# Optimization experiments

Hardware: AMD Instinct MI355X
Metric: run time of the kernel (lower is better)

The kernel has to match this reference:

```python
import jax, jax.numpy as jnp
import numpy as np

N, E, D, H, LAYERS = 50000, 800000, 128, 8, 2
LRELU_ALPHA = 0.2


def _seg_softmax(logits, seg, n):
    # numerically stable softmax over edges grouped by destination node
    m = jax.ops.segment_max(logits, seg, num_segments=n)
    z = jnp.exp(logits - m[seg])
    s = jax.ops.segment_sum(z, seg, num_segments=n)
    return z / jnp.maximum(s[seg], 1e-16)


def _gat_layer(x, src, dst, W, a_src, a_dst, concat):
    # W: [H, Fin, F'], a_src/a_dst: [H, F']
    n = x.shape[0]
    outs = []
    for h in range(W.shape[0]):  # loop over heads to bound peak memory
        Wh = x @ W[h]                              # [N, F']
        es = Wh @ a_src[h]                         # [N]
        ed = Wh @ a_dst[h]                         # [N]
        e = jax.nn.leaky_relu(es[src] + ed[dst], LRELU_ALPHA)  # [E]
        att = _seg_softmax(e, dst, n)              # [E]
        out = jax.ops.segment_sum(att[:, None] * Wh[src], dst, num_segments=n)
        outs.append(out)
    if concat:
        return jax.nn.elu(jnp.concatenate(outs, axis=-1))  # [N, H*F']
    return jnp.mean(jnp.stack(outs, axis=0), axis=0)        # [N, F']


def _rel_gcn_layer(x, src, dst, w, W):
    # weighted-adjacency GCN with row (in-degree) normalization + ReLU
    n = x.shape[0]
    deg = jax.ops.segment_sum(w, dst, num_segments=n)
    norm = w / jnp.maximum(deg[dst], 1e-16)        # [E]
    h = x @ W                                      # [N, Dout]
    agg = jax.ops.segment_sum(norm[:, None] * h[src], dst, num_segments=n)
    return jax.nn.relu(agg)


def setup_inputs() -> dict:
    key = jax.random.key(0)
    ks = jax.random.split(key, 12)
    s = 1.0 / np.sqrt(D)
    return {
        "x": jax.random.normal(ks[0], (N, D), dtype=jnp.float32),
        "edge_index": jax.random.randint(ks[1], (2, E), 0, N, dtype=jnp.int64),
        "edge_weight": jax.random.uniform(ks[2], (E,), dtype=jnp.float32),
        "gat_W0": jax.random.normal(ks[3], (H, D, D // H), dtype=jnp.float32) * s,
        "gat_a0_src": jax.random.normal(ks[4], (H, D // H), dtype=jnp.float32) * s,
        "gat_a0_dst": jax.random.normal(ks[5], (H, D // H), dtype=jnp.float32) * s,
        "gat_W1": jax.random.normal(ks[6], (H, D, D), dtype=jnp.float32) * s,
        "gat_a1_src": jax.random.normal(ks[7], (H, D), dtype=jnp.float32) * s,
        "gat_a1_dst": jax.random.normal(ks[8], (H, D), dtype=jnp.float32) * s,
        "gcn_W0": jax.random.normal(ks[9], (D, D), dtype=jnp.float32) * s,
        "gcn_W1": jax.random.normal(ks[10], (D, D), dtype=jnp.float32) * s,
    }


def reference(x, edge_index, edge_weight, gat_W0, gat_a0_src, gat_a0_dst,
              gat_W1, gat_a1_src, gat_a1_dst, gcn_W0, gcn_W1):
    src, dst = edge_index[0], edge_index[1]
    gat_params = [(gat_W0, gat_a0_src, gat_a0_dst), (gat_W1, gat_a1_src, gat_a1_dst)]
    gcn_params = [gcn_W0, gcn_W1]
    x1, x2 = x, x  # dropout is identity in eval mode
    for i in range(LAYERS):
        W, a_s, a_d = gat_params[i]
        x1 = _gat_layer(x1, src, dst, W, a_s, a_d, concat=(i != LAYERS - 1))
        x2 = _rel_gcn_layer(x2, src, dst, edge_weight, gcn_params[i])
    # cat along new last dim then MaxPool1d(2) == elementwise max of branches
    return jnp.maximum(x1, x2)
```

## Files before the change

kernel.cpp:

```cpp
#include <hip/hip_runtime.h>

#define LRELU_ALPHA 0.2f

typedef __attribute__((ext_vector_type(8))) short short8;
typedef __attribute__((ext_vector_type(4))) float float4v;
typedef __attribute__((ext_vector_type(2))) float f32x2;

__device__ __forceinline__ unsigned short f2bf(float f) {
  union { float f; unsigned u; } x; x.f = f;
  unsigned r = (x.u + 0x7fff + ((x.u >> 16) & 1)) >> 16;
  return (unsigned short)r;
}
__device__ __forceinline__ float bflo(unsigned u) {
  union { unsigned u; float f; } x; x.u = u << 16; return x.f;
}
__device__ __forceinline__ float bfhi(unsigned u) {
  union { unsigned u; float f; } x; x.u = u & 0xffff0000u; return x.f;
}
__device__ __forceinline__ f32x2 bfpair(unsigned u) {
  return (f32x2){bflo(u), bfhi(u)};
}


__global__ __launch_bounds__(256) void k_count(const int* __restrict__ dst,
                                               int* __restrict__ cnt, int E) {
  int e = blockIdx.x * 256 + threadIdx.x;
  if (e < E) atomicAdd(&cnt[dst[e]], 1);
}

__global__ __launch_bounds__(1024) void k_scan1(const int* __restrict__ cnt,
                                                int* __restrict__ lscan,
                                                int* __restrict__ bsum, int N) {
  __shared__ int sm[1024];
  int t = threadIdx.x;
  int base = blockIdx.x * 1024;
  int v = (base + t < N) ? cnt[base + t] : 0;
  sm[t] = v;
  __syncthreads();
  for (int off = 1; off < 1024; off <<= 1) {
    int x = (t >= off) ? sm[t - off] : 0;
    __syncthreads();
    sm[t] += x;
    __syncthreads();
  }
  if (base + t < N) lscan[base + t] = sm[t] - v;
  if (t == 1023) bsum[blockIdx.x] = sm[1023];
}

__global__ __launch_bounds__(64) void k_scan2(int* __restrict__ bsum,
                                              int* __restrict__ rowptrN, int nb) {
  int t = threadIdx.x;
  int v = (t < nb) ? bsum[t] : 0;
  int orig = v;
  for (int off = 1; off < 64; off <<= 1) {
    int y = __shfl_up(v, off, 64);
    if (t >= off) v += y;
  }
  if (t < nb) bsum[t] = v - orig;
  if (t == 63) *rowptrN = v;
}

__global__ __launch_bounds__(1024) void k_scan3(int* __restrict__ rowptr,
                                                int* __restrict__ cur,
                                                const int* __restrict__ bsum, int N) {
  int i = blockIdx.x * 1024 + threadIdx.x;
  if (i < N) {
    int v = rowptr[i] + bsum[blockIdx.x];
    rowptr[i] = v;
    cur[i] = v;
  }
}

__global__ __launch_bounds__(256) void k_scatter(const int* __restrict__ src,
                                                 const int* __restrict__ dst,
                                                 const float* __restrict__ w,
                                                 int* __restrict__ cur,
                                                 uint2* __restrict__ edata, int E) {
  int e = blockIdx.x * 256 + threadIdx.x;
  if (e < E) {
    int d = dst[e];
    int p = atomicAdd(&cur[d], 1);
    edata[p] = make_uint2((unsigned)src[e], __float_as_uint(w[e]));
  }
}

__global__ __launch_bounds__(256) void k_pack(const float* __restrict__ W0,
                                              const float* __restrict__ a0s,
                                              const float* __restrict__ a0d,
                                              const float* __restrict__ W1,
                                              const float* __restrict__ a1s,
                                              const float* __restrict__ a1d,
                                              const float* __restrict__ gw0,
                                              const float* __restrict__ gw1,
                                              unsigned short* __restrict__ W0catT,
                                              float* __restrict__ logitW,
                                              unsigned short* __restrict__ gw1T,
                                              unsigned short* __restrict__ va1T,
                                              unsigned short* __restrict__ WstackT) {
  int idx = blockIdx.x * 256 + threadIdx.x;
  if (idx < 32768) {
    int n = idx >> 7, k = idx & 127;
    int q = n >> 2, r = n & 3;
    float v;
    if (r < 2) {
      int o = 2 * q + r;
      int h = o >> 4, f = o & 15;
      v = W0[h * 2048 + k * 16 + f];
    } else {
      int j = 2 * q + (r - 2);
      v = gw0[k * 128 + j];
    }
    W0catT[idx] = f2bf(v);
  } else if (idx < 34816) {
    int j = idx - 32768;
    int k = j >> 4, c = j & 15;
    int h = (c < 8) ? c : c - 8;
    const float* a = (c < 8) ? a0s : a0d;
    float s = 0.f;
    for (int f = 0; f < 16; ++f) s += W0[h * 2048 + k * 16 + f] * a[h * 16 + f];
    logitW[j] = s;
  } else if (idx < 51200) {
    int j = idx - 34816;
    int n = j >> 7, k = j & 127;
    gw1T[j] = f2bf(gw1[k * 128 + n]);
  } else if (idx < 53248) {
    int j = idx - 51200;
    int c = j >> 7, k = j & 127;
    int h = c & 7;
    const float* a = (c < 8) ? a1s : a1d;
    float s = 0.f;
    for (int f = 0; f < 128; ++f) s += W1[h * 16384 + k * 128 + f] * a[h * 128 + f];
    va1T[j] = f2bf(s);
  } else if (idx < 184320) {
    int j = idx - 53248;
    int n = j >> 10, kk = j & 1023;
    int h = kk >> 7, k = kk & 127;
    WstackT[j] = f2bf(W1[h * 16384 + k * 128 + n] * 0.125f);
  }
}

__global__ __launch_bounds__(256) void k_prep(const float* __restrict__ x,
                                              const float* __restrict__ logitW,
                                              unsigned short* __restrict__ xb,
                                              float* __restrict__ logit0, int N) {
  __shared__ float sm[16][132];
  __shared__ float sw[2048];
  int t = threadIdx.x;
  int base = blockIdx.x * 16;
  int r = t >> 4, cc = (t & 15) * 8;
  const float* xr = x + (size_t)(base + r) * 128 + cc;
  float4 v0 = *(const float4*)xr;
  float4 v1 = *(const float4*)(xr + 4);
  ushort4 o0 = {f2bf(v0.x), f2bf(v0.y), f2bf(v0.z), f2bf(v0.w)};
  ushort4 o1 = {f2bf(v1.x), f2bf(v1.y), f2bf(v1.z), f2bf(v1.w)};
  *(ushort4*)(xb + (size_t)(base + r) * 128 + cc) = o0;
  *(ushort4*)(xb + (size_t)(base + r) * 128 + cc + 4) = o1;
  *(float4*)&sm[r][cc] = v0;
  *(float4*)&sm[r][cc + 4] = v1;
  *(float4*)&sw[t * 8] = *(const float4*)(logitW + t * 8);
  *(float4*)&sw[t * 8 + 4] = *(const float4*)(logitW + t * 8 + 4);
  __syncthreads();
  int c = t & 15;
  float acc = 0.f;
#pragma unroll
  for (int k = 0; k < 128; ++k) acc += sm[r][k] * sw[k * 16 + c];
  logit0[(size_t)(base + r) * 16 + c] = acc;
}

__global__ __launch_bounds__(256) void k_pedge(const float* __restrict__ logits,
                                               const uint2* __restrict__ edata,
                                               const int* __restrict__ rowptr,
                                               unsigned short* __restrict__ pedge,
                                               float* __restrict__ linv, int N) {
  int wave = threadIdx.x >> 6, lane = threadIdx.x & 63;
  int d = blockIdx.x * 4 + wave;
  if (d >= N) return;
  int j8 = lane >> 3, h = lane & 7;
  float edv = logits[(size_t)d * 16 + 8 + h];
  int beg = rowptr[d], end = rowptr[d + 1];
  float lsum = 0.f;
  for (int ii = beg + j8; ii < end; ii += 8) {
    unsigned s = edata[ii].x;
    float es = logits[(size_t)s * 16 + h];
    float lg = es + edv;
    lg = lg > 0.f ? lg : LRELU_ALPHA * lg;
    float p = __expf(fminf(lg, 80.f));
    lsum += p;
    pedge[(size_t)ii * 8 + h] = f2bf(p);
  }
  lsum += __shfl_xor(lsum, 8, 64);
  lsum += __shfl_xor(lsum, 16, 64);
  lsum += __shfl_xor(lsum, 32, 64);
  if (lane < 8) linv[(size_t)d * 8 + h] = lsum > 0.f ? 1.f / lsum : 0.f;
}

template <int NT, int OUT_BF16, int EPI>
__global__ __launch_bounds__(256) void k_mgemm(const unsigned short* __restrict__ A, int lda,
                                               const unsigned short* __restrict__ BT, int ldb,
                                               void* __restrict__ Cv, int ldc,
                                               const void* __restrict__ aux,
                                               int M, int Ncols, int K) {
  __shared__ unsigned short As[64][64];
  __shared__ unsigned short Bs[NT * 16][64];
  int tid = threadIdx.x;
  int w = tid >> 6, lane = tid & 63;
  int quad = lane >> 4, l16 = lane & 15;
  int row0 = blockIdx.x * 64;
  int c0 = blockIdx.y * (NT * 16);
  float4v acc[NT];
#pragma unroll
  for (int t = 0; t < NT; ++t) acc[t] = (float4v){0.f, 0.f, 0.f, 0.f};

  for (int k0 = 0; k0 < K; k0 += 64) {
    __syncthreads();
#pragma unroll
    for (int i = 0; i < 2; ++i) {
      int c = tid + i * 256;
      int r = c >> 3, kc = c & 7;
      uint4 v = {0u, 0u, 0u, 0u};
      int gr = row0 + r;
      if (gr < M) v = *(const uint4*)(A + (size_t)gr * lda + k0 + kc * 8);
      *(uint4*)(&As[r][(kc ^ (r & 7)) * 8]) = v;
    }
#pragma unroll
    for (int i = 0; i < (NT * 128 + 255) / 256; ++i) {
      int c = tid + i * 256;
      if (c < NT * 128) {
        int n = c >> 3, kc = c & 7;
        uint4 v = {0u, 0u, 0u, 0u};
        int gn = c0 + n;
        if (gn < Ncols) v = *(const uint4*)(BT + (size_t)gn * ldb + k0 + kc * 8);
        *(uint4*)(&Bs[n][(kc ^ (n & 7)) * 8]) = v;
      }
    }
    __syncthreads();
#pragma unroll
    for (int ks = 0; ks < 2; ++ks) {
      int m = w * 16 + l16;
      int ga = (ks * 4 + quad) ^ (m & 7);
      short8 a = *(const short8*)(&As[m][ga * 8]);
#pragma unroll
      for (int t = 0; t < NT; ++t) {
        int n = t * 16 + l16;
        int gb = (ks * 4 + quad) ^ (n & 7);
        short8 b = *(const short8*)(&Bs[n][gb * 8]);
        acc[t] = __builtin_amdgcn_mfma_f32_16x16x32_bf16(a, b, acc[t], 0, 0, 0);
      }
    }
  }
#pragma unroll
  for (int t = 0; t < NT; ++t) {
    int cc = c0 + t * 16 + l16;
    if (cc >= Ncols) continue;
#pragma unroll
    for (int i = 0; i < 4; ++i) {
      int rr = row0 + w * 16 + quad * 4 + i;
      if (rr >= M) continue;
      float v = acc[t][i];
      if (EPI == 1) {
        unsigned short us = ((const unsigned short*)aux)[(size_t)rr * ldc + cc];
        v = fmaxf(v, bflo((unsigned)us));
      }
      if (EPI == 2) {
        ((unsigned short*)Cv)[(size_t)rr * 256 + 4 * (cc >> 1) + 2 + (cc & 1)] = f2bf(v);
      } else if (OUT_BF16)
        ((unsigned short*)Cv)[(size_t)rr * ldc + cc] = f2bf(v);
      else
        ((float*)Cv)[(size_t)rr * ldc + cc] = v;
    }
  }
}

__global__ __launch_bounds__(256) void k_agg0(const unsigned short* __restrict__ feat0i,
                                              const int* __restrict__ rowptr,
                                              const uint2* __restrict__ edata,
                                              const unsigned short* __restrict__ pedge,
                                              const float* __restrict__ linv,
                                              unsigned short* __restrict__ x1c,
                                              unsigned short* __restrict__ x2,
                                              unsigned short* __restrict__ xh, int N) {
  __shared__ uint2 swl[4][64];
  __shared__ float pl[4][512];
  int wave = threadIdx.x >> 6, lane = threadIdx.x & 63;
  int d = blockIdx.x * 4 + wave;
  if (d >= N) return;
  int head = lane >> 3;
  int beg = rowptr[d], end = rowptr[d + 1], deg = end - beg;
  float wsum = 0.f;
  f32x2 a2 = {0.f, 0.f}, g2 = {0.f, 0.f};
  for (int base = 0; base < deg; base += 64) {
    int idx = beg + base + lane;
    bool valid = idx < end;
    uint2 sv = make_uint2(0u, 0u);
    float4 pa = {0.f, 0.f, 0.f, 0.f}, pb = {0.f, 0.f, 0.f, 0.f};
    if (valid) {
      sv = edata[idx];
      ushort4 q0 = *(const ushort4*)(pedge + (size_t)idx * 8);
      ushort4 q1 = *(const ushort4*)(pedge + (size_t)idx * 8 + 4);
      pa = make_float4(bflo(q0.x), bflo(q0.y), bflo(q0.z), bflo(q0.w));
      pb = make_float4(bflo(q1.x), bflo(q1.y), bflo(q1.z), bflo(q1.w));
    }
    swl[wave][lane] = sv;
    *(float4*)&pl[wave][lane * 8] = pa;
    *(float4*)&pl[wave][lane * 8 + 4] = pb;
    int ng = deg - base; if (ng > 64) ng = 64;
    int groups = (ng + 7) >> 3;
    for (int g = 0; g < groups; ++g) {
#pragma unroll
      for (int j = 0; j < 8; ++j) {
        int e = g * 8 + j;
        uint2 sw = swl[wave][e];
        float pj = pl[wave][e * 8 + head];
        float wj = __uint_as_float(sw.y);
        uint2 u = *(const uint2*)(feat0i + (size_t)sw.x * 256 + 4 * lane);
        a2 += bfpair(u.x) * pj;
        g2 += bfpair(u.y) * wj;
        wsum += wj;
      }
    }
  }
  float inv = linv[(size_t)d * 8 + head];
  float v0 = a2.x * inv, v1 = a2.y * inv;
  v0 = v0 > 0.f ? v0 : __expf(v0) - 1.f;
  v1 = v1 > 0.f ? v1 : __expf(v1) - 1.f;
  unsigned xpack = (unsigned)f2bf(v0) | ((unsigned)f2bf(v1) << 16);
  ((unsigned*)x1c)[(size_t)d * 64 + lane] = xpack;
  ((unsigned*)xh)[(size_t)d * 128 + 2 * lane] = xpack;
  float ginv = 1.f / fmaxf(wsum, 1e-16f);
  float w0 = fmaxf(g2.x * ginv, 0.f), w1 = fmaxf(g2.y * ginv, 0.f);
  ((unsigned*)x2)[(size_t)d * 64 + lane] = (unsigned)f2bf(w0) | ((unsigned)f2bf(w1) << 16);
}

__global__ __launch_bounds__(256) void k_agg1(const unsigned short* __restrict__ xh,
                                              const int* __restrict__ rowptr,
                                              const uint2* __restrict__ edata,
                                              const unsigned short* __restrict__ pedge,
                                              const float* __restrict__ linv,
                                              unsigned short* __restrict__ aggbuf,
                                              unsigned short* __restrict__ x2f,
                                              int d0, int d1) {
  __shared__ uint2 swl[4][64];
  __shared__ float pl[4][512];
  int wave = threadIdx.x >> 6, lane = threadIdx.x & 63;
  int d = d0 + blockIdx.x * 4 + wave;
  if (d >= d1) return;
  int beg = rowptr[d], end = rowptr[d + 1], deg = end - beg;
  f32x2 ax2[8] = {};
  f32x2 g2 = {0.f, 0.f};
  float wsum = 0.f;
  for (int base = 0; base < deg; base += 64) {
    int idx = beg + base + lane;
    bool valid = idx < end;
    uint2 sv = make_uint2(0u, 0u);
    float4 pa = {0.f, 0.f, 0.f, 0.f}, pb = {0.f, 0.f, 0.f, 0.f};
    if (valid) {
      sv = edata[idx];
      ushort4 q0 = *(const ushort4*)(pedge + (size_t)idx * 8);
      ushort4 q1 = *(const ushort4*)(pedge + (size_t)idx * 8 + 4);
      pa = make_float4(bflo(q0.x), bflo(q0.y), bflo(q0.z), bflo(q0.w));
      pb = make_float4(bflo(q1.x), bflo(q1.y), bflo(q1.z), bflo(q1.w));
    }
    swl[wave][lane] = sv;
    *(float4*)&pl[wave][lane * 8] = pa;
    *(float4*)&pl[wave][lane * 8 + 4] = pb;
    int ng = deg - base; if (ng > 64) ng = 64;
    int groups = (ng + 7) >> 3;
    for (int g = 0; g < groups; ++g) {
#pragma unroll
      for (int j = 0; j < 8; ++j) {
        int e = g * 8 + j;
        uint2 sw = swl[wave][e];
        float4 pv0 = *(const float4*)&pl[wave][e * 8];
        float4 pv1 = *(const float4*)&pl[wave][e * 8 + 4];
        uint2 u = *(const uint2*)(xh + (size_t)sw.x * 256 + 4 * lane);
        f32x2 xv = bfpair(u.x);
        float wj = __uint_as_float(sw.y);
        g2 += bfpair(u.y) * wj;
        wsum += wj;
        ax2[0] += xv * pv0.x;
        ax2[1] += xv * pv0.y;
        ax2[2] += xv * pv0.z;
        ax2[3] += xv * pv0.w;
        ax2[4] += xv * pv1.x;
        ax2[5] += xv * pv1.y;
        ax2[6] += xv * pv1.z;
        ax2[7] += xv * pv1.w;
      }
    }
  }
  float4 i0 = *(const float4*)(linv + (size_t)d * 8);
  float4 i1 = *(const float4*)(linv + (size_t)d * 8 + 4);
  float invh[8] = {i0.x, i0.y, i0.z, i0.w, i1.x, i1.y, i1.z, i1.w};
  size_t lr = (size_t)(d - d0) * 512;
#pragma unroll
  for (int h = 0; h < 8; ++h) {
    ((unsigned*)aggbuf)[lr + h * 64 + lane] =
        (unsigned)f2bf(ax2[h].x * invh[h]) | ((unsigned)f2bf(ax2[h].y * invh[h]) << 16);
  }
  float ginv = 1.f / fmaxf(wsum, 1e-16f);
  float w0 = fmaxf(g2.x * ginv, 0.f), w1 = fmaxf(g2.y * ginv, 0.f);
  ((unsigned*)x2f)[(size_t)d * 64 + lane] = (unsigned)f2bf(w0) | ((unsigned)f2bf(w1) << 16);
}


extern "C" void kernel_launch(void* const* d_in, const int* in_sizes, int n_in,
                              void* d_out, int out_size, void* d_ws, size_t ws_size,
                              hipStream_t stream) {
  const float* x   = (const float*)d_in[0];
  const int*   ei  = (const int*)d_in[1];
  const float* ew  = (const float*)d_in[2];
  const float* W0  = (const float*)d_in[3];
  const float* a0s = (const float*)d_in[4];
  const float* a0d = (const float*)d_in[5];
  const float* W1  = (const float*)d_in[6];
  const float* a1s = (const float*)d_in[7];
  const float* a1d = (const float*)d_in[8];
  const float* gw0 = (const float*)d_in[9];
  const float* gw1 = (const float*)d_in[10];
  float* out = (float*)d_out;

  const int N = in_sizes[0] / 128;
  const int E = in_sizes[1] / 2;
  const int* src = ei;
  const int* dst = ei + E;

  char* p = (char*)d_ws;
  auto carve = [&](size_t bytes) {
    void* r = (void*)p;
    p += (bytes + 255) & ~(size_t)255;
    return r;
  };
  int*   cnt    = (int*)carve((size_t)N * 4);
  int*   rowptr = (int*)carve((size_t)(N + 1) * 4);
  int*   cur    = (int*)carve((size_t)N * 4);
  int*   bsum   = (int*)carve(256 * 4);
  uint2* edata  = (uint2*)carve((size_t)E * 8);
  unsigned short* W0catT  = (unsigned short*)carve(32768 * 2);
  float*          logitW  = (float*)carve(2048 * 4);
  unsigned short* gw1T    = (unsigned short*)carve(16384 * 2);
  unsigned short* va1T    = (unsigned short*)carve(2048 * 2);
  unsigned short* WstackT = (unsigned short*)carve(131072 * 2);
  unsigned short* x1c  = (unsigned short*)carve((size_t)N * 128 * 2);
  unsigned short* x2   = (unsigned short*)carve((size_t)N * 128 * 2);
  unsigned short* x2f  = (unsigned short*)carve((size_t)N * 128 * 2);
  float*          esed = (float*)carve((size_t)N * 16 * 4);
  unsigned short* xh   = (unsigned short*)carve((size_t)N * 256 * 2);
  unsigned short* pedge = (unsigned short*)carve((size_t)E * 8 * 2);
  float*          linv0 = (float*)carve((size_t)N * 8 * 4);
  float*          linv1 = (float*)carve((size_t)N * 8 * 4);
  const int CH = 25600;
  size_t ph1 = ((size_t)N * 128 * 2 + 255) & ~(size_t)255;
  size_t ph2 = ph1 + (((size_t)N * 256 * 2 + 255) & ~(size_t)255);
  size_t ph3 = ph2 + (((size_t)N * 16 * 4 + 255) & ~(size_t)255);
  size_t scratch_sz = (size_t)CH * 1024 * 2;
  if (ph3 > scratch_sz) scratch_sz = ph3;
  char* scratch = (char*)carve(scratch_sz);
  unsigned short* xb     = (unsigned short*)scratch;
  unsigned short* feat0i = (unsigned short*)(scratch + ph1);
  float*          logit0 = (float*)(scratch + ph2);
  unsigned short* aggbuf = (unsigned short*)scratch;

  hipMemsetAsync(cnt, 0, (size_t)N * 4, stream);
  int gE = (E + 255) / 256;
  k_count<<<gE, 256, 0, stream>>>(dst, cnt, E);
  int nb = (N + 1023) / 1024;
  k_scan1<<<nb, 1024, 0, stream>>>(cnt, rowptr, bsum, N);
  k_scan2<<<1, 64, 0, stream>>>(bsum, rowptr + N, nb);
  k_scan3<<<nb, 1024, 0, stream>>>(rowptr, cur, bsum, N);
  k_scatter<<<gE, 256, 0, stream>>>(src, dst, ew, cur, edata, E);

  k_pack<<<(184320 + 255) / 256, 256, 0, stream>>>(W0, a0s, a0d, W1, a1s, a1d, gw0,
                                                   gw1, W0catT, logitW, gw1T, va1T,
                                                   WstackT);
  k_prep<<<(N + 15) / 16, 256, 0, stream>>>(x, logitW, xb, logit0, N);

  int gM = (N + 63) / 64;
  int gD = (N + 3) / 4;
  k_mgemm<8, 1, 0><<<dim3(gM, 2), 256, 0, stream>>>(xb, 128, W0catT, 128, feat0i, 256,
                                                    nullptr, N, 256, 128);
  k_pedge<<<gD, 256, 0, stream>>>(logit0, edata, rowptr, pedge, linv0, N);
  k_agg0<<<gD, 256, 0, stream>>>(feat0i, rowptr, edata, pedge, linv0, x1c, x2, xh, N);

  k_mgemm<1, 0, 0><<<dim3(gM, 1), 256, 0, stream>>>(x1c, 128, va1T, 128, esed, 16,
                                                    nullptr, N, 16, 128);
  k_mgemm<8, 1, 2><<<dim3(gM, 1), 256, 0, stream>>>(x2, 128, gw1T, 128, xh, 256,
                                                    nullptr, N, 128, 128);

  k_pedge<<<gD, 256, 0, stream>>>(esed, edata, rowptr, pedge, linv1, N);

  for (int d0 = 0; d0 < N; d0 += CH) {
    int d1 = d0 + CH < N ? d0 + CH : N;
    int chN = d1 - d0;
    k_agg1<<<(chN + 3) / 4, 256, 0, stream>>>(xh, rowptr, edata, pedge, linv1,
                                              aggbuf, x2f, d0, d1);
    k_mgemm<8, 0, 1><<<dim3((chN + 63) / 64, 1), 256, 0, stream>>>(
        aggbuf, 1024, WstackT, 1024, out + (size_t)d0 * 128, 128,
        x2f + (size_t)d0 * 128, chN, 128, 1024);
  }
}
```

Measured before the change: 502.7 us.

## Fuse layer-0 edge logits into scatter, drop max-subtraction, split edges across half-waves

```diff
diff --git a/kernel.cpp b/kernel.cpp
--- a/kernel.cpp
+++ b/kernel.cpp
@@ -19,6 +19,9 @@
 }
 __device__ __forceinline__ f32x2 bfpair(unsigned u) {
   return (f32x2){bflo(u), bfhi(u)};
+}
+__device__ __forceinline__ unsigned packbf(float a, float b) {
+  return (unsigned)f2bf(a) | ((unsigned)f2bf(b) << 16);
 }
 
 
@@ -74,14 +77,33 @@
 __global__ __launch_bounds__(256) void k_scatter(const int* __restrict__ src,
                                                  const int* __restrict__ dst,
                                                  const float* __restrict__ w,
+                                                 const float* __restrict__ logit0,
                                                  int* __restrict__ cur,
-                                                 uint2* __restrict__ edata, int E) {
+                                                 uint2* __restrict__ edata,
+                                                 unsigned short* __restrict__ pedge,
+                                                 int E) {
   int e = blockIdx.x * 256 + threadIdx.x;
-  if (e < E) {
-    int d = dst[e];
-    int p = atomicAdd(&cur[d], 1);
-    edata[p] = make_uint2((unsigned)src[e], __float_as_uint(w[e]));
-  }
+  if (e >= E) return;
+  int d = dst[e];
+  int s = src[e];
+  int p = atomicAdd(&cur[d], 1);
+  edata[p] = make_uint2((unsigned)s, __float_as_uint(w[e]));
+  float4 es0 = *(const float4*)(logit0 + (size_t)s * 16);
+  float4 es1 = *(const float4*)(logit0 + (size_t)s * 16 + 4);
+  float4 ed0 = *(const float4*)(logit0 + (size_t)d * 16 + 8);
+  float4 ed1 = *(const float4*)(logit0 + (size_t)d * 16 + 12);
+  float lg[8] = {es0.x + ed0.x, es0.y + ed0.y, es0.z + ed0.z, es0.w + ed0.w,
+                 es1.x + ed1.x, es1.y + ed1.y, es1.z + ed1.z, es1.w + ed1.w};
+  unsigned short o[8];
+#pragma unroll
+  for (int h = 0; h < 8; ++h) {
+    float v = lg[h] > 0.f ? lg[h] : LRELU_ALPHA * lg[h];
+    o[h] = f2bf(__expf(fminf(v, 80.f)));
+  }
+  ushort4 q0 = {o[0], o[1], o[2], o[3]};
+  ushort4 q1 = {o[4], o[5], o[6], o[7]};
+  *(ushort4*)(pedge + (size_t)p * 8) = q0;
+  *(ushort4*)(pedge + (size_t)p * 8 + 4) = q1;
 }
 
 __global__ __launch_bounds__(256) void k_pack(const float* __restrict__ W0,
@@ -275,7 +297,6 @@
                                               const int* __restrict__ rowptr,
                                               const uint2* __restrict__ edata,
                                               const unsigned short* __restrict__ pedge,
-                                              const float* __restrict__ linv,
                                               unsigned short* __restrict__ x1c,
                                               unsigned short* __restrict__ x2,
                                               unsigned short* __restrict__ xh, int N) {
@@ -284,51 +305,62 @@
   int wave = threadIdx.x >> 6, lane = threadIdx.x & 63;
   int d = blockIdx.x * 4 + wave;
   if (d >= N) return;
-  int head = lane >> 3;
+  int half = lane >> 5, lane2 = lane & 31;
+  int head = lane2 >> 2;
   int beg = rowptr[d], end = rowptr[d + 1], deg = end - beg;
-  float wsum = 0.f;
-  f32x2 a2 = {0.f, 0.f}, g2 = {0.f, 0.f};
+  f32x2 aa = {0.f, 0.f}, ab = {0.f, 0.f}, ga = {0.f, 0.f}, gb = {0.f, 0.f};
+  float l = 0.f, wsum = 0.f;
   for (int base = 0; base < deg; base += 64) {
     int idx = beg + base + lane;
-    bool valid = idx < end;
     uint2 sv = make_uint2(0u, 0u);
-    float4 pa = {0.f, 0.f, 0.f, 0.f}, pb = {0.f, 0.f, 0.f, 0.f};
-    if (valid) {
+    uint4 q = make_uint4(0u, 0u, 0u, 0u);
+    if (idx < end) {
       sv = edata[idx];
-      ushort4 q0 = *(const ushort4*)(pedge + (size_t)idx * 8);
-      ushort4 q1 = *(const ushort4*)(pedge + (size_t)idx * 8 + 4);
-      pa = make_float4(bflo(q0.x), bflo(q0.y), bflo(q0.z), bflo(q0.w));
-      pb = make_float4(bflo(q1.x), bflo(q1.y), bflo(q1.z), bflo(q1.w));
+      q = *(const uint4*)(pedge + (size_t)idx * 8);
     }
     swl[wave][lane] = sv;
+    float4 pa = make_float4(bflo(q.x), bfhi(q.x), bflo(q.y), bfhi(q.y));
+    float4 pb = make_float4(bflo(q.z), bfhi(q.z), bflo(q.w), bfhi(q.w));
     *(float4*)&pl[wave][lane * 8] = pa;
     *(float4*)&pl[wave][lane * 8 + 4] = pb;
     int ng = deg - base; if (ng > 64) ng = 64;
-    int groups = (ng + 7) >> 3;
-    for (int g = 0; g < groups; ++g) {
-#pragma unroll
-      for (int j = 0; j < 8; ++j) {
-        int e = g * 8 + j;
-        uint2 sw = swl[wave][e];
-        float pj = pl[wave][e * 8 + head];
-        float wj = __uint_as_float(sw.y);
-        uint2 u = *(const uint2*)(feat0i + (size_t)sw.x * 256 + 4 * lane);
-        a2 += bfpair(u.x) * pj;
-        g2 += bfpair(u.y) * wj;
-        wsum += wj;
-      }
-    }
-  }
-  float inv = linv[(size_t)d * 8 + head];
-  float v0 = a2.x * inv, v1 = a2.y * inv;
-  v0 = v0 > 0.f ? v0 : __expf(v0) - 1.f;
-  v1 = v1 > 0.f ? v1 : __expf(v1) - 1.f;
-  unsigned xpack = (unsigned)f2bf(v0) | ((unsigned)f2bf(v1) << 16);
-  ((unsigned*)x1c)[(size_t)d * 64 + lane] = xpack;
-  ((unsigned*)xh)[(size_t)d * 128 + 2 * lane] = xpack;
-  float ginv = 1.f / fmaxf(wsum, 1e-16f);
-  float w0 = fmaxf(g2.x * ginv, 0.f), w1 = fmaxf(g2.y * ginv, 0.f);
-  ((unsigned*)x2)[(size_t)d * 64 + lane] = (unsigned)f2bf(w0) | ((unsigned)f2bf(w1) << 16);
+    int tp = (ng + 1) >> 1;
+    for (int t = 0; t < tp; ++t) {
+      int e = 2 * t + half;
+      uint2 sw = swl[wave][e];
+      float p = pl[wave][e * 8 + head];
+      float wj = __uint_as_float(sw.y);
+      uint4 u = *(const uint4*)(feat0i + (size_t)sw.x * 256 + 8 * lane2);
+      aa += bfpair(u.x) * p;
+      ga += bfpair(u.y) * wj;
+      ab += bfpair(u.z) * p;
+      gb += bfpair(u.w) * wj;
+      l += p;
+      wsum += wj;
+    }
+  }
+  aa.x += __shfl_xor(aa.x, 32, 64); aa.y += __shfl_xor(aa.y, 32, 64);
+  ab.x += __shfl_xor(ab.x, 32, 64); ab.y += __shfl_xor(ab.y, 32, 64);
+  ga.x += __shfl_xor(ga.x, 32, 64); ga.y += __shfl_xor(ga.y, 32, 64);
+  gb.x += __shfl_xor(gb.x, 32, 64); gb.y += __shfl_xor(gb.y, 32, 64);
+  l += __shfl_xor(l, 32, 64);
+  wsum += __shfl_xor(wsum, 32, 64);
+  if (half == 0) {
+    float inv = l > 0.f ? 1.f / l : 0.f;
+    float v0 = aa.x * inv, v1 = aa.y * inv, v2 = ab.x * inv, v3 = ab.y * inv;
+    v0 = v0 > 0.f ? v0 : __expf(v0) - 1.f;
+    v1 = v1 > 0.f ? v1 : __expf(v1) - 1.f;
+    v2 = v2 > 0.f ? v2 : __expf(v2) - 1.f;
+    v3 = v3 > 0.f ? v3 : __expf(v3) - 1.f;
+    unsigned p0 = packbf(v0, v1), p1 = packbf(v2, v3);
+    ((uint2*)x1c)[(size_t)d * 32 + lane2] = make_uint2(p0, p1);
+    ((unsigned*)xh)[(size_t)d * 128 + 4 * lane2] = p0;
+    ((unsigned*)xh)[(size_t)d * 128 + 4 * lane2 + 2] = p1;
+    float ginv = 1.f / fmaxf(wsum, 1e-16f);
+    float w0 = fmaxf(ga.x * ginv, 0.f), w1 = fmaxf(ga.y * ginv, 0.f);
+    float w2 = fmaxf(gb.x * ginv, 0.f), w3 = fmaxf(gb.y * ginv, 0.f);
+    ((uint2*)x2)[(size_t)d * 32 + lane2] = make_uint2(packbf(w0, w1), packbf(w2, w3));
+  }
 }
 
 __global__ __launch_bounds__(256) void k_agg1(const unsigned short* __restrict__ xh,
@@ -344,62 +376,72 @@
   int wave = threadIdx.x >> 6, lane = threadIdx.x & 63;
   int d = d0 + blockIdx.x * 4 + wave;
   if (d >= d1) return;
+  int half = lane >> 5, lane2 = lane & 31;
   int beg = rowptr[d], end = rowptr[d + 1], deg = end - beg;
-  f32x2 ax2[8] = {};
-  f32x2 g2 = {0.f, 0.f};
+  f32x2 axA[8] = {}, axB[8] = {};
+  f32x2 ga = {0.f, 0.f}, gb = {0.f, 0.f};
   float wsum = 0.f;
   for (int base = 0; base < deg; base += 64) {
     int idx = beg + base + lane;
-    bool valid = idx < end;
     uint2 sv = make_uint2(0u, 0u);
-    float4 pa = {0.f, 0.f, 0.f, 0.f}, pb = {0.f, 0.f, 0.f, 0.f};
-    if (valid) {
+    uint4 q = make_uint4(0u, 0u, 0u, 0u);
+    if (idx < end) {
       sv = edata[idx];
-      ushort4 q0 = *(const ushort4*)(pedge + (size_t)idx * 8);
-      ushort4 q1 = *(const ushort4*)(pedge + (size_t)idx * 8 + 4);
-      pa = make_float4(bflo(q0.x), bflo(q0.y), bflo(q0.z), bflo(q0.w));
-      pb = make_float4(bflo(q1.x), bflo(q1.y), bflo(q1.z), bflo(q1.w));
+      q = *(const uint4*)(pedge + (size_t)idx * 8);
     }
     swl[wave][lane] = sv;
+    float4 pa = make_float4(bflo(q.x), bfhi(q.x), bflo(q.y), bfhi(q.y));
+    float4 pb = make_float4(bflo(q.z), bfhi(q.z), bflo(q.w), bfhi(q.w));
     *(float4*)&pl[wave][lane * 8] = pa;
     *(float4*)&pl[wave][lane * 8 + 4] = pb;
     int ng = deg - base; if (ng > 64) ng = 64;
-    int groups = (ng + 7) >> 3;
-    for (int g = 0; g < groups; ++g) {
-#pragma unroll
-      for (int j = 0; j < 8; ++j) {
-        int e = g * 8 + j;
-        uint2 sw = swl[wave][e];
-        float4 pv0 = *(const float4*)&pl[wave][e * 8];
-        float4 pv1 = *(const float4*)&pl[wave][e * 8 + 4];
-        uint2 u = *(const uint2*)(xh + (size_t)sw.x * 256 + 4 * lane);
-        f32x2 xv = bfpair(u.x);
-        float wj = __uint_as_float(sw.y);
-        g2 += bfpair(u.y) * wj;
-        wsum += wj;
-        ax2[0] += xv * pv0.x;
-        ax2[1] += xv * pv0.y;
-        ax2[2] += xv * pv0.z;
-        ax2[3] += xv * pv0.w;
-        ax2[4] += xv * pv1.x;
-        ax2[5] += xv * pv1.y;
-        ax2[6] += xv * pv1.z;
-        ax2[7] += xv * pv1.w;
-      }
-    }
-  }
-  float4 i0 = *(const float4*)(linv + (size_t)d * 8);
-  float4 i1 = *(const float4*)(linv + (size_t)d * 8 + 4);
-  float invh[8] = {i0.x, i0.y, i0.z, i0.w, i1.x, i1.y, i1.z, i1.w};
-  size_t lr = (size_t)(d - d0) * 512;
+    int tp = (ng + 1) >> 1;
+    for (int t = 0; t < tp; ++t) {
+      int e = 2 * t + half;
+      uint2 sw = swl[wave][e];
+      float4 pv0 = *(const float4*)&pl[wave][e * 8];
+      float4 pv1 = *(const float4*)&pl[wave][e * 8 + 4];
+      float wj = __uint_as_float(sw.y);
+      uint4 u = *(const uint4*)(xh + (size_t)sw.x * 256 + 8 * lane2);
+      f32x2 xA = bfpair(u.x), hA = bfpair(u.y);
+      f32x2 xB = bfpair(u.z), hB = bfpair(u.w);
+      ga += hA * wj;
+      gb += hB * wj;
+      wsum += wj;
+      axA[0] += xA * pv0.x; axB[0] += xB * pv0.x;
+      axA[1] += xA * pv0.y; axB[1] += xB * pv0.y;
+      axA[2] += xA * pv0.z; axB[2] += xB * pv0.z;
+      axA[3] += xA * pv0.w; axB[3] += xB * pv0.w;
+      axA[4] += xA * pv1.x; axB[4] += xB * pv1.x;
+      axA[5] += xA * pv1.y; axB[5] += xB * pv1.y;
+      axA[6] += xA * pv1.z; axB[6] += xB * pv1.z;
+      axA[7] += xA * pv1.w; axB[7] += xB * pv1.w;
+    }
+  }
 #pragma unroll
   for (int h = 0; h < 8; ++h) {
-    ((unsigned*)aggbuf)[lr + h * 64 + lane] =
-        (unsigned)f2bf(ax2[h].x * invh[h]) | ((unsigned)f2bf(ax2[h].y * invh[h]) << 16);
-  }
-  float ginv = 1.f / fmaxf(wsum, 1e-16f);
-  float w0 = fmaxf(g2.x * ginv, 0.f), w1 = fmaxf(g2.y * ginv, 0.f);
-  ((unsigned*)x2f)[(size_t)d * 64 + lane] = (unsigned)f2bf(w0) | ((unsigned)f2bf(w1) << 16);
+    axA[h].x += __shfl_xor(axA[h].x, 32, 64); axA[h].y += __shfl_xor(axA[h].y, 32, 64);
+    axB[h].x += __shfl_xor(axB[h].x, 32, 64); axB[h].y += __shfl_xor(axB[h].y, 32, 64);
+  }
+  ga.x += __shfl_xor(ga.x, 32, 64); ga.y += __shfl_xor(ga.y, 32, 64);
+  gb.x += __shfl_xor(gb.x, 32, 64); gb.y += __shfl_xor(gb.y, 32, 64);
+  wsum += __shfl_xor(wsum, 32, 64);
+  if (half == 0) {
+    float4 i0 = *(const float4*)(linv + (size_t)d * 8);
+    float4 i1 = *(const float4*)(linv + (size_t)d * 8 + 4);
+    float invh[8] = {i0.x, i0.y, i0.z, i0.w, i1.x, i1.y, i1.z, i1.w};
+    size_t lr2 = (size_t)(d - d0) * 256;
+#pragma unroll
+    for (int h = 0; h < 8; ++h) {
+      ((uint2*)aggbuf)[lr2 + h * 32 + lane2] =
+          make_uint2(packbf(axA[h].x * invh[h], axA[h].y * invh[h]),
+                     packbf(axB[h].x * invh[h], axB[h].y * invh[h]));
+    }
+    float ginv = 1.f / fmaxf(wsum, 1e-16f);
+    float w0 = fmaxf(ga.x * ginv, 0.f), w1 = fmaxf(ga.y * ginv, 0.f);
+    float w2 = fmaxf(gb.x * ginv, 0.f), w3 = fmaxf(gb.y * ginv, 0.f);
+    ((uint2*)x2f)[(size_t)d * 32 + lane2] = make_uint2(packbf(w0, w1), packbf(w2, w3));
+  }
 }
 
 
@@ -446,7 +488,6 @@
   float*          esed = (float*)carve((size_t)N * 16 * 4);
   unsigned short* xh   = (unsigned short*)carve((size_t)N * 256 * 2);
   unsigned short* pedge = (unsigned short*)carve((size_t)E * 8 * 2);
-  float*          linv0 = (float*)carve((size_t)N * 8 * 4);
   float*          linv1 = (float*)carve((size_t)N * 8 * 4);
   const int CH = 25600;
   size_t ph1 = ((size_t)N * 128 * 2 + 255) & ~(size_t)255;
@@ -460,26 +501,27 @@
   float*          logit0 = (float*)(scratch + ph2);
   unsigned short* aggbuf = (unsigned short*)scratch;
 
+  int gE = (E + 255) / 256;
+  int nb = (N + 1023) / 1024;
+  int gM = (N + 63) / 64;
+  int gD = (N + 3) / 4;
+
   hipMemsetAsync(cnt, 0, (size_t)N * 4, stream);
-  int gE = (E + 255) / 256;
   k_count<<<gE, 256, 0, stream>>>(dst, cnt, E);
-  int nb = (N + 1023) / 1024;
   k_scan1<<<nb, 1024, 0, stream>>>(cnt, rowptr, bsum, N);
   k_scan2<<<1, 64, 0, stream>>>(bsum, rowptr + N, nb);
   k_scan3<<<nb, 1024, 0, stream>>>(rowptr, cur, bsum, N);
-  k_scatter<<<gE, 256, 0, stream>>>(src, dst, ew, cur, edata, E);
 
   k_pack<<<(184320 + 255) / 256, 256, 0, stream>>>(W0, a0s, a0d, W1, a1s, a1d, gw0,
                                                    gw1, W0catT, logitW, gw1T, va1T,
                                                    WstackT);
   k_prep<<<(N + 15) / 16, 256, 0, stream>>>(x, logitW, xb, logit0, N);
 
-  int gM = (N + 63) / 64;
-  int gD = (N + 3) / 4;
+  k_scatter<<<gE, 256, 0, stream>>>(src, dst, ew, logit0, cur, edata, pedge, E);
+
   k_mgemm<8, 1, 0><<<dim3(gM, 2), 256, 0, stream>>>(xb, 128, W0catT, 128, feat0i, 256,
                                                     nullptr, N, 256, 128);
-  k_pedge<<<gD, 256, 0, stream>>>(logit0, edata, rowptr, pedge, linv0, N);
-  k_agg0<<<gD, 256, 0, stream>>>(feat0i, rowptr, edata, pedge, linv0, x1c, x2, xh, N);
+  k_agg0<<<gD, 256, 0, stream>>>(feat0i, rowptr, edata, pedge, x1c, x2, xh, N);
 
   k_mgemm<1, 0, 0><<<dim3(gM, 1), 256, 0, stream>>>(x1c, 128, va1T, 128, esed, 16,
                                                     nullptr, N, 16, 128);
```

Result: faster. 492.3 us (-2.1%).
